# Optimization experiments

Measured on AMD Instinct MI355X. Metric: run time of the kernel, lower is better.

The kernel has to match this reference:

```python
import jax, jax.numpy as jnp
import numpy as np

N = 8192
IN_DIM = 512
OUT_DIM = 256
ALPHA = 0.2  # LeakyReLU negative slope


def setup_inputs() -> dict:
    key = jax.random.key(0)
    k_nodes, k_edge, k_W, k_Wb, k_a1, k_a1b, k_a2, k_a2b = jax.random.split(key, 8)
    nodes = jax.random.normal(k_nodes, (N, IN_DIM), dtype=jnp.float32)
    edge_mat = jax.random.uniform(k_edge, (N, N)) > 0.5
    edge_mat = edge_mat | jnp.eye(N, dtype=bool)
    s_W = 1.0 / np.sqrt(IN_DIM)
    s_a = 1.0 / np.sqrt(OUT_DIM)
    W_w = jax.random.uniform(k_W, (OUT_DIM, IN_DIM), minval=-s_W, maxval=s_W, dtype=jnp.float32)
    W_b = jax.random.uniform(k_Wb, (OUT_DIM,), minval=-s_W, maxval=s_W, dtype=jnp.float32)
    a1_w = jax.random.uniform(k_a1, (1, OUT_DIM), minval=-s_a, maxval=s_a, dtype=jnp.float32)
    a1_b = jax.random.uniform(k_a1b, (1,), minval=-s_a, maxval=s_a, dtype=jnp.float32)
    a2_w = jax.random.uniform(k_a2, (1, OUT_DIM), minval=-s_a, maxval=s_a, dtype=jnp.float32)
    a2_b = jax.random.uniform(k_a2b, (1,), minval=-s_a, maxval=s_a, dtype=jnp.float32)
    return {"nodes": nodes, "edge_mat": edge_mat, "W_w": W_w, "W_b": W_b,
            "a1_w": a1_w, "a1_b": a1_b, "a2_w": a2_w, "a2_b": a2_b}


def reference(nodes, edge_mat, W_w, W_b, a1_w, a1_b, a2_w, a2_b):
    Wh = nodes @ W_w.T + W_b                      # [N, OUT_DIM]
    Wh1 = Wh @ a1_w.T + a1_b                      # [N, 1]
    Wh2 = Wh @ a2_w.T + a2_b                      # [N, 1]
    scores = jax.nn.leaky_relu(Wh1 + Wh2.T, negative_slope=ALPHA)  # [N, N]
    masked = jnp.where(edge_mat, scores, -jnp.inf)
    attention = jax.nn.softmax(masked, axis=1)    # [N, N]
    return attention @ Wh                         # [N, OUT_DIM]
```

## Files before the change

kernel.cpp:

```cpp
#include <hip/hip_runtime.h>
#include <hip/hip_bf16.h>
#include <stdint.h>


#define NN 8192
#define IND 512
#define OUTD 256

typedef __attribute__((ext_vector_type(8))) short short8;
typedef __attribute__((ext_vector_type(4))) short short4v;
typedef __attribute__((ext_vector_type(4))) float f32x4;
typedef __attribute__((ext_vector_type(4))) int i32x4;
typedef __attribute__((ext_vector_type(4))) unsigned int u32x4;

#define AS_GLOBAL __attribute__((address_space(1)))
#define AS_LDS __attribute__((address_space(3)))

static __device__ __forceinline__ short f2bf(float f) {
  return __builtin_bit_cast(short, __float2bfloat16(f));
}

extern "C" __global__ __launch_bounds__(256) void k_convert_w(
    const float* __restrict__ W, short* __restrict__ W2) {
  const int t = blockIdx.x * 256 + threadIdx.x;
  const int row = t >> 6, kb = t & 63;
  const float* src = W + row * IND + kb * 8;
  f32x4 x0 = *(const f32x4*)src;
  f32x4 x1 = *(const f32x4*)(src + 4);
  short8 o;
  o[0] = f2bf(x0[0]); o[1] = f2bf(x0[1]); o[2] = f2bf(x0[2]); o[3] = f2bf(x0[3]);
  o[4] = f2bf(x1[0]); o[5] = f2bf(x1[1]); o[6] = f2bf(x1[2]); o[7] = f2bf(x1[3]);
  *(short8*)(W2 + (size_t)kb * 2048 + row * 8) = o;
}

extern "C" __global__ __launch_bounds__(128) void k_wh(
    const float* __restrict__ nodes, const short* __restrict__ W2,
    const float* __restrict__ Wb, const float* __restrict__ a1w,
    const float* __restrict__ a1b, const float* __restrict__ a2w,
    const float* __restrict__ a2b, short* __restrict__ WhL,
    float* __restrict__ s1, float* __restrict__ sAC,
    uint32_t* __restrict__ sPK) {
  const int tid = threadIdx.x;
  const int wv = tid >> 6, lane = tid & 63, g = lane >> 4, m = lane & 15;
  const int rowbase = blockIdx.x * 32 + wv * 16;

  f32x4 acc[16];
#pragma unroll
  for (int nf = 0; nf < 16; ++nf) acc[nf] = (f32x4){0.f, 0.f, 0.f, 0.f};

  const float* arow = nodes + (size_t)(rowbase + m) * IND;
  const short* bb = W2 + (size_t)g * 2048 + m * 8;
#pragma unroll 4
  for (int k0 = 0; k0 < IND; k0 += 32) {
    const float* ap = arow + k0 + g * 8;
    f32x4 x0 = *(const f32x4*)ap;
    f32x4 x1 = *(const f32x4*)(ap + 4);
    short8 af;
    af[0] = f2bf(x0[0]); af[1] = f2bf(x0[1]); af[2] = f2bf(x0[2]); af[3] = f2bf(x0[3]);
    af[4] = f2bf(x1[0]); af[5] = f2bf(x1[1]); af[6] = f2bf(x1[2]); af[7] = f2bf(x1[3]);
    const short* bk = bb + (size_t)(k0 >> 3) * 2048;
#pragma unroll
    for (int nf = 0; nf < 16; ++nf) {
      short8 bf = *(const short8*)(bk + nf * 128);
      acc[nf] = __builtin_amdgcn_mfma_f32_16x16x32_bf16(af, bf, acc[nf], 0, 0, 0);
    }
  }

  float p1[4] = {0.f, 0.f, 0.f, 0.f}, p2[4] = {0.f, 0.f, 0.f, 0.f};
#pragma unroll
  for (int nf = 0; nf < 16; ++nf) {
    const int n = nf * 16 + m;
    const float b = Wb[n], c1 = a1w[n], c2 = a2w[n];
#pragma unroll
    for (int r = 0; r < 4; ++r) {
      float v = acc[nf][r] + b;
      acc[nf][r] = v;
      p1[r] += c1 * v;
      p2[r] += c2 * v;
    }
  }
#pragma unroll
  for (int off = 1; off < 16; off <<= 1) {
#pragma unroll
    for (int r = 0; r < 4; ++r) {
      p1[r] += __shfl_xor(p1[r], off);
      p2[r] += __shfl_xor(p2[r], off);
    }
  }
  if (m == 0) {
    const float b1 = a1b[0], b2 = a2b[0];
#pragma unroll
    for (int r = 0; r < 4; ++r) {
      const int row = rowbase + g * 4 + r;
      const float v1 = p1[r] + b1, v2 = p2[r] + b2;
      s1[row] = v1;
      sAC[row] = __expf(v1);
      sAC[NN + row] = __expf(0.2f * v1);
      const float B = __expf(v2), D = __expf(0.2f * v2);
      sPK[2 * row] = __builtin_bit_cast(uint32_t, B);
      sPK[2 * row + 1] =
          ((uint32_t)(uint16_t)f2bf(D) << 16) | (uint16_t)f2bf(v2);
    }
  }

  const size_t cbase = ((size_t)(rowbase >> 3) + (g >> 1)) * 2048 + (g & 1) * 4;
#pragma unroll
  for (int nf = 0; nf < 16; ++nf) {
    short4v o;
#pragma unroll
    for (int r = 0; r < 4; ++r) o[r] = f2bf(acc[nf][r]);
    *(short4v*)(WhL + cbase + (size_t)(nf * 16 + m) * 8) = o;
  }
}

extern "C" __global__ __launch_bounds__(512, 4) void k_attn(
    const int* __restrict__ mask, const short* __restrict__ WhL,
    const float* __restrict__ s1, const float* __restrict__ sAC,
    const uint32_t* __restrict__ sPK,
    float* __restrict__ pnum, float* __restrict__ pden) {
  __shared__ char smem[51200];
  uint32_t* PKs = (uint32_t*)(smem + 32768);
  char* Ms = smem + 40960;

  const int tid = threadIdx.x;
  const int w = tid >> 6, lane = tid & 63, g = lane >> 4, m = lane & 15;
  const int rt = blockIdx.x >> 3, jc = blockIdx.x & 7;
  const int rg = w & 3, ns = w >> 2;
  const int rb = rt * 128 + rg * 32;

  const float T0 = -s1[rb + m],        T1 = -s1[rb + 16 + m];
  const float A0 = sAC[rb + m],        A1 = sAC[rb + 16 + m];
  const float C0 = sAC[NN + rb + m],   C1 = sAC[NN + rb + 16 + m];

  f32x4 acc0[8], acc1[8];
#pragma unroll
  for (int nf = 0; nf < 8; ++nf) {
    acc0[nf] = (f32x4){0.f, 0.f, 0.f, 0.f};
    acc1[nf] = (f32x4){0.f, 0.f, 0.f, 0.f};
  }
  float den0 = 0.f, den1 = 0.f;

  const int rloc = tid >> 2, jq = tid & 3;
  const int* msrc = mask + (size_t)(rt * 128 + rloc) * NN + jc * 1024 + jq * 8;
  const int mwr = rloc * 40 + jq * 8;
  const int mrow0 = (rg * 32 + m) * 40 + g * 8;
  const int mrow1 = (rg * 32 + 16 + m) * 40 + g * 8;
  const short* gS = WhL + (size_t)jc * 262144;

  auto pack8 = [](const i32x4& a, const i32x4& b) -> uint64_t {
    uint64_t p = 0;
    p |= (a[0] != 0) ? 1ull : 0;
    p |= (a[1] != 0) ? (1ull << 8) : 0;
    p |= (a[2] != 0) ? (1ull << 16) : 0;
    p |= (a[3] != 0) ? (1ull << 24) : 0;
    p |= (b[0] != 0) ? (1ull << 32) : 0;
    p |= (b[1] != 0) ? (1ull << 40) : 0;
    p |= (b[2] != 0) ? (1ull << 48) : 0;
    p |= (b[3] != 0) ? (1ull << 56) : 0;
    return p;
  };

  auto build = [&](float T, float A, float C, uint64_t pb,
                   const u32x4& q0, const u32x4& q1,
                   const u32x4& q2, const u32x4& q3, float& den) -> short8 {
    const uint32_t Bv[8] = {q0[0], q0[2], q1[0], q1[2],
                            q2[0], q2[2], q3[0], q3[2]};
    const uint32_t Dv[8] = {q0[1], q0[3], q1[1], q1[3],
                            q2[1], q2[3], q3[1], q3[3]};
    short8 af;
#pragma unroll
    for (int i = 0; i < 8; ++i) {
      const float s2v = __builtin_bit_cast(float, Dv[i] << 16);
      const bool pos = s2v > T;
      const float wv = __builtin_bit_cast(float, pos ? Bv[i] : (Dv[i] & 0xFFFF0000u));
      const float a = pos ? A : C;
      const float val = wv * a;
      const float pv = ((pb >> (8 * i)) & 1) ? val : 0.f;
      den += pv;
      af[i] = f2bf(pv);
    }
    return af;
  };

  i32x4 mA0 = __builtin_nontemporal_load((const i32x4*)msrc);
  i32x4 mA1 = __builtin_nontemporal_load((const i32x4*)(msrc + 4));
  __builtin_amdgcn_global_load_lds(
      (const AS_GLOBAL void*)((const char*)sPK + (size_t)jc * 8192 + tid * 16),
      (AS_LDS void*)(smem + 32768 + tid * 16), 16, 0, 0);
  __builtin_amdgcn_global_load_lds((const AS_GLOBAL void*)(gS + tid * 8),
                                   (AS_LDS void*)(smem + tid * 16), 16, 0, 0);
  __builtin_amdgcn_global_load_lds((const AS_GLOBAL void*)(gS + 4096 + tid * 8),
                                   (AS_LDS void*)(smem + 8192 + tid * 16), 16, 0, 0);
  *(uint64_t*)(Ms + mwr) = pack8(mA0, mA1);
  i32x4 mB0 = __builtin_nontemporal_load((const i32x4*)(msrc + 32));
  i32x4 mB1 = __builtin_nontemporal_load((const i32x4*)(msrc + 36));
  asm volatile("s_waitcnt vmcnt(2)" ::: "memory");
  __builtin_amdgcn_sched_barrier(0);
  asm volatile("s_waitcnt lgkmcnt(0)" ::: "memory");
  __builtin_amdgcn_s_barrier();

  auto body = [&](int u, i32x4& is0, i32x4& is1, i32x4& cs0, i32x4& cs1) {
    const int wn = (u + 2 < 32) ? u + 2 : 31;
    is0 = __builtin_nontemporal_load((const i32x4*)(msrc + wn * 32));
    is1 = __builtin_nontemporal_load((const i32x4*)(msrc + wn * 32 + 4));
    const int us = (u + 1 < 32) ? u + 1 : 31;
    {
      const short* gsl = gS + us * 8192 + tid * 8;
      char* dst = smem + ((u + 1) & 1) * 16384 + tid * 16;
      __builtin_amdgcn_global_load_lds((const AS_GLOBAL void*)gsl,
                                       (AS_LDS void*)dst, 16, 0, 0);
      __builtin_amdgcn_global_load_lds((const AS_GLOBAL void*)(gsl + 4096),
                                       (AS_LDS void*)(dst + 8192), 16, 0, 0);
    }
    asm volatile("s_waitcnt vmcnt(4)" ::: "memory");
    __builtin_amdgcn_sched_barrier(0);
    if (u < 31) *(uint64_t*)(Ms + ((u + 1) & 1) * 5120 + mwr) = pack8(cs0, cs1);
    const uint64_t pb0 = *(const uint64_t*)(Ms + (u & 1) * 5120 + mrow0);
    const uint64_t pb1 = *(const uint64_t*)(Ms + (u & 1) * 5120 + mrow1);
    const uint32_t* pk = &PKs[u * 64 + g * 16];
    const u32x4 q0 = *(const u32x4*)(pk + 0);
    const u32x4 q1 = *(const u32x4*)(pk + 4);
    const u32x4 q2 = *(const u32x4*)(pk + 8);
    const u32x4 q3 = *(const u32x4*)(pk + 12);
    short8 af0 = build(T0, A0, C0, pb0, q0, q1, q2, q3, den0);
    short8 af1 = build(T1, A1, C1, pb1, q0, q1, q2, q3, den1);
    const short* bl = (const short*)(smem + (u & 1) * 16384) +
                      g * 2048 + (ns * 128 + m) * 8;
#pragma unroll
    for (int nf = 0; nf < 8; ++nf) {
      short8 bf = *(const short8*)(bl + nf * 128);
      acc0[nf] = __builtin_amdgcn_mfma_f32_16x16x32_bf16(af0, bf, acc0[nf], 0, 0, 0);
      acc1[nf] = __builtin_amdgcn_mfma_f32_16x16x32_bf16(af1, bf, acc1[nf], 0, 0, 0);
    }
    asm volatile("s_waitcnt lgkmcnt(0)" ::: "memory");
    __builtin_amdgcn_s_barrier();
  };

  for (int uu = 0; uu < 32; uu += 2) {
    body(uu, mA0, mA1, mB0, mB1);
    body(uu + 1, mB0, mB1, mA0, mA1);
  }

  den0 += __shfl_xor(den0, 16); den0 += __shfl_xor(den0, 32);
  den1 += __shfl_xor(den1, 16); den1 += __shfl_xor(den1, 32);
  if (ns == 0 && lane < 16) {
    pden[jc * NN + rb + m] = den0;
    pden[jc * NN + rb + 16 + m] = den1;
  }

  float* pn = pnum + (size_t)jc * NN * OUTD + (size_t)rb * OUTD + ns * 128;
#pragma unroll
  for (int r = 0; r < 4; ++r) {
    const int q = g * 4 + r;
#pragma unroll
    for (int nf = 0; nf < 8; ++nf) {
      pn[(size_t)q * OUTD + nf * 16 + m] = acc0[nf][r];
      pn[(size_t)(16 + q) * OUTD + nf * 16 + m] = acc1[nf][r];
    }
  }
}

extern "C" __global__ __launch_bounds__(256) void k_comb(
    const float* __restrict__ pnum, const float* __restrict__ pden,
    float* __restrict__ out) {
  const int idx = blockIdx.x * 256 + threadIdx.x;
  const int row = idx >> 6, c4 = (idx & 63) * 4;
  f32x4 s = (f32x4){0.f, 0.f, 0.f, 0.f};
  float d = 0.f;
#pragma unroll
  for (int jc = 0; jc < 8; ++jc) {
    f32x4 v = *(const f32x4*)(pnum + ((size_t)jc * NN + row) * OUTD + c4);
    s += v;
    d += pden[jc * NN + row];
  }
  const float inv = 1.f / d;
  *(f32x4*)(out + (size_t)row * OUTD + c4) = s * inv;
}

extern "C" void kernel_launch(void* const* d_in, const int* in_sizes, int n_in,
                              void* d_out, int out_size, void* d_ws, size_t ws_size,
                              hipStream_t stream) {
  const float* nodes = (const float*)d_in[0];
  const int*   mask  = (const int*)d_in[1];
  const float* W_w   = (const float*)d_in[2];
  const float* W_b   = (const float*)d_in[3];
  const float* a1w   = (const float*)d_in[4];
  const float* a1b   = (const float*)d_in[5];
  const float* a2w   = (const float*)d_in[6];
  const float* a2b   = (const float*)d_in[7];
  float* out = (float*)d_out;

  char* ws = (char*)d_ws;
  short*    WhL  = (short*)(ws);
  float*    s1   = (float*)(ws + (size_t)4  * 1024 * 1024);
  short*    W2   = (short*)(ws + (size_t)4  * 1024 * 1024 + 65536);
  float*    sAC  = (float*)(ws + (size_t)13 * 1024 * 1024);
  uint32_t* sPK  = (uint32_t*)(ws + (size_t)14 * 1024 * 1024);
  float*    pnum = (float*)(ws + (size_t)16 * 1024 * 1024);
  float*    pden = (float*)(ws + (size_t)96 * 1024 * 1024);

  hipLaunchKernelGGL(k_convert_w, dim3(64), dim3(256), 0, stream, W_w, W2);
  hipLaunchKernelGGL(k_wh, dim3(256), dim3(128), 0, stream,
                     nodes, W2, W_b, a1w, a1b, a2w, a2b, WhL, s1, sAC, sPK);
  hipLaunchKernelGGL(k_attn, dim3(512), dim3(512), 0, stream,
                     mask, WhL, s1, sAC, sPK, pnum, pden);
  hipLaunchKernelGGL(k_comb, dim3(2048), dim3(256), 0, stream,
                     pnum, pden, out);
}
```

Baseline: 198.6 us.

## Halve attention row tile and read mask directly into registers, drop LDS mask packing

The attention kernel now covers 64 rows per block instead of 128, with one 16-row MFMA fragment per wave. The grid doubles to 1024 blocks. Each lane loads its own mask ints straight from global memory into registers, which removes the LDS bit-packing stage and its extra barrier wait. The mask prefetch moves after the MFMAs, and the MFMA section runs at raised wave priority. The cost is that each block reads its WhL tiles from LDS for half as many rows, so WhL global/LDS traffic per output roughly doubles, and the mask loads are less coalesced.

```diff
diff --git a/kernel.cpp b/kernel.cpp
--- a/kernel.cpp
+++ b/kernel.cpp
@@ -118,51 +118,30 @@
     const float* __restrict__ s1, const float* __restrict__ sAC,
     const uint32_t* __restrict__ sPK,
     float* __restrict__ pnum, float* __restrict__ pden) {
-  __shared__ char smem[51200];
+  __shared__ char smem[40960];
   uint32_t* PKs = (uint32_t*)(smem + 32768);
-  char* Ms = smem + 40960;
 
   const int tid = threadIdx.x;
   const int w = tid >> 6, lane = tid & 63, g = lane >> 4, m = lane & 15;
   const int rt = blockIdx.x >> 3, jc = blockIdx.x & 7;
   const int rg = w & 3, ns = w >> 2;
-  const int rb = rt * 128 + rg * 32;
-
-  const float T0 = -s1[rb + m],        T1 = -s1[rb + 16 + m];
-  const float A0 = sAC[rb + m],        A1 = sAC[rb + 16 + m];
-  const float C0 = sAC[NN + rb + m],   C1 = sAC[NN + rb + 16 + m];
-
-  f32x4 acc0[8], acc1[8];
-#pragma unroll
-  for (int nf = 0; nf < 8; ++nf) {
-    acc0[nf] = (f32x4){0.f, 0.f, 0.f, 0.f};
-    acc1[nf] = (f32x4){0.f, 0.f, 0.f, 0.f};
-  }
-  float den0 = 0.f, den1 = 0.f;
-
-  const int rloc = tid >> 2, jq = tid & 3;
-  const int* msrc = mask + (size_t)(rt * 128 + rloc) * NN + jc * 1024 + jq * 8;
-  const int mwr = rloc * 40 + jq * 8;
-  const int mrow0 = (rg * 32 + m) * 40 + g * 8;
-  const int mrow1 = (rg * 32 + 16 + m) * 40 + g * 8;
+  const int rb = rt * 64 + rg * 16;
+
+  const float T0 = -s1[rb + m];
+  const float A0 = sAC[rb + m];
+  const float C0 = sAC[NN + rb + m];
+
+  f32x4 acc[8];
+#pragma unroll
+  for (int nf = 0; nf < 8; ++nf) acc[nf] = (f32x4){0.f, 0.f, 0.f, 0.f};
+  float den = 0.f;
+
+  const int* mr = mask + (size_t)(rb + m) * NN + jc * 1024 + g * 8;
   const short* gS = WhL + (size_t)jc * 262144;
 
-  auto pack8 = [](const i32x4& a, const i32x4& b) -> uint64_t {
-    uint64_t p = 0;
-    p |= (a[0] != 0) ? 1ull : 0;
-    p |= (a[1] != 0) ? (1ull << 8) : 0;
-    p |= (a[2] != 0) ? (1ull << 16) : 0;
-    p |= (a[3] != 0) ? (1ull << 24) : 0;
-    p |= (b[0] != 0) ? (1ull << 32) : 0;
-    p |= (b[1] != 0) ? (1ull << 40) : 0;
-    p |= (b[2] != 0) ? (1ull << 48) : 0;
-    p |= (b[3] != 0) ? (1ull << 56) : 0;
-    return p;
-  };
-
-  auto build = [&](float T, float A, float C, uint64_t pb,
+  auto build = [&](const i32x4& lo, const i32x4& hi,
                    const u32x4& q0, const u32x4& q1,
-                   const u32x4& q2, const u32x4& q3, float& den) -> short8 {
+                   const u32x4& q2, const u32x4& q3) -> short8 {
     const uint32_t Bv[8] = {q0[0], q0[2], q1[0], q1[2],
                             q2[0], q2[2], q3[0], q3[2]};
     const uint32_t Dv[8] = {q0[1], q0[3], q1[1], q1[3],
@@ -171,19 +150,22 @@
 #pragma unroll
     for (int i = 0; i < 8; ++i) {
       const float s2v = __builtin_bit_cast(float, Dv[i] << 16);
-      const bool pos = s2v > T;
+      const bool pos = s2v > T0;
       const float wv = __builtin_bit_cast(float, pos ? Bv[i] : (Dv[i] & 0xFFFF0000u));
-      const float a = pos ? A : C;
+      const float a = pos ? A0 : C0;
       const float val = wv * a;
-      const float pv = ((pb >> (8 * i)) & 1) ? val : 0.f;
+      const int mv = (i < 4) ? lo[i] : hi[i - 4];
+      const float pv = (mv != 0) ? val : 0.f;
       den += pv;
       af[i] = f2bf(pv);
     }
     return af;
   };
 
-  i32x4 mA0 = __builtin_nontemporal_load((const i32x4*)msrc);
-  i32x4 mA1 = __builtin_nontemporal_load((const i32x4*)(msrc + 4));
+  i32x4 mA0 = __builtin_nontemporal_load((const i32x4*)mr);
+  i32x4 mA1 = __builtin_nontemporal_load((const i32x4*)(mr + 4));
+  i32x4 mB0 = __builtin_nontemporal_load((const i32x4*)(mr + 32));
+  i32x4 mB1 = __builtin_nontemporal_load((const i32x4*)(mr + 36));
   __builtin_amdgcn_global_load_lds(
       (const AS_GLOBAL void*)((const char*)sPK + (size_t)jc * 8192 + tid * 16),
       (AS_LDS void*)(smem + 32768 + tid * 16), 16, 0, 0);
@@ -191,20 +173,12 @@
                                    (AS_LDS void*)(smem + tid * 16), 16, 0, 0);
   __builtin_amdgcn_global_load_lds((const AS_GLOBAL void*)(gS + 4096 + tid * 8),
                                    (AS_LDS void*)(smem + 8192 + tid * 16), 16, 0, 0);
-  *(uint64_t*)(Ms + mwr) = pack8(mA0, mA1);
-  i32x4 mB0 = __builtin_nontemporal_load((const i32x4*)(msrc + 32));
-  i32x4 mB1 = __builtin_nontemporal_load((const i32x4*)(msrc + 36));
-  asm volatile("s_waitcnt vmcnt(2)" ::: "memory");
-  __builtin_amdgcn_sched_barrier(0);
-  asm volatile("s_waitcnt lgkmcnt(0)" ::: "memory");
+  asm volatile("s_waitcnt vmcnt(0)" ::: "memory");
   __builtin_amdgcn_s_barrier();
 
-  auto body = [&](int u, i32x4& is0, i32x4& is1, i32x4& cs0, i32x4& cs1) {
-    const int wn = (u + 2 < 32) ? u + 2 : 31;
-    is0 = __builtin_nontemporal_load((const i32x4*)(msrc + wn * 32));
-    is1 = __builtin_nontemporal_load((const i32x4*)(msrc + wn * 32 + 4));
-    const int us = (u + 1 < 32) ? u + 1 : 31;
+  auto body = [&](int u, i32x4& c0, i32x4& c1) {
     {
+      const int us = (u + 1 < 32) ? u + 1 : 31;
       const short* gsl = gS + us * 8192 + tid * 8;
       char* dst = smem + ((u + 1) & 1) * 16384 + tid * 16;
       __builtin_amdgcn_global_load_lds((const AS_GLOBAL void*)gsl,
@@ -214,39 +188,37 @@
     }
     asm volatile("s_waitcnt vmcnt(4)" ::: "memory");
     __builtin_amdgcn_sched_barrier(0);
-    if (u < 31) *(uint64_t*)(Ms + ((u + 1) & 1) * 5120 + mwr) = pack8(cs0, cs1);
-    const uint64_t pb0 = *(const uint64_t*)(Ms + (u & 1) * 5120 + mrow0);
-    const uint64_t pb1 = *(const uint64_t*)(Ms + (u & 1) * 5120 + mrow1);
     const uint32_t* pk = &PKs[u * 64 + g * 16];
     const u32x4 q0 = *(const u32x4*)(pk + 0);
     const u32x4 q1 = *(const u32x4*)(pk + 4);
     const u32x4 q2 = *(const u32x4*)(pk + 8);
     const u32x4 q3 = *(const u32x4*)(pk + 12);
-    short8 af0 = build(T0, A0, C0, pb0, q0, q1, q2, q3, den0);
-    short8 af1 = build(T1, A1, C1, pb1, q0, q1, q2, q3, den1);
+    short8 af = build(c0, c1, q0, q1, q2, q3);
     const short* bl = (const short*)(smem + (u & 1) * 16384) +
                       g * 2048 + (ns * 128 + m) * 8;
+    __builtin_amdgcn_s_setprio(1);
 #pragma unroll
     for (int nf = 0; nf < 8; ++nf) {
       short8 bf = *(const short8*)(bl + nf * 128);
-      acc0[nf] = __builtin_amdgcn_mfma_f32_16x16x32_bf16(af0, bf, acc0[nf], 0, 0, 0);
-      acc1[nf] = __builtin_amdgcn_mfma_f32_16x16x32_bf16(af1, bf, acc1[nf], 0, 0, 0);
-    }
-    asm volatile("s_waitcnt lgkmcnt(0)" ::: "memory");
+      acc[nf] = __builtin_amdgcn_mfma_f32_16x16x32_bf16(af, bf, acc[nf], 0, 0, 0);
+    }
+    __builtin_amdgcn_s_setprio(0);
+    {
+      const int wn = (u + 2 < 32) ? u + 2 : 31;
+      c0 = __builtin_nontemporal_load((const i32x4*)(mr + wn * 32));
+      c1 = __builtin_nontemporal_load((const i32x4*)(mr + wn * 32 + 4));
+    }
     __builtin_amdgcn_s_barrier();
   };
 
   for (int uu = 0; uu < 32; uu += 2) {
-    body(uu, mA0, mA1, mB0, mB1);
-    body(uu + 1, mB0, mB1, mA0, mA1);
-  }
-
-  den0 += __shfl_xor(den0, 16); den0 += __shfl_xor(den0, 32);
-  den1 += __shfl_xor(den1, 16); den1 += __shfl_xor(den1, 32);
-  if (ns == 0 && lane < 16) {
-    pden[jc * NN + rb + m] = den0;
-    pden[jc * NN + rb + 16 + m] = den1;
-  }
+    body(uu, mA0, mA1);
+    body(uu + 1, mB0, mB1);
+  }
+
+  den += __shfl_xor(den, 16);
+  den += __shfl_xor(den, 32);
+  if (ns == 0 && lane < 16) pden[jc * NN + rb + m] = den;
 
   float* pn = pnum + (size_t)jc * NN * OUTD + (size_t)rb * OUTD + ns * 128;
 #pragma unroll
@@ -254,8 +226,7 @@
     const int q = g * 4 + r;
 #pragma unroll
     for (int nf = 0; nf < 8; ++nf) {
-      pn[(size_t)q * OUTD + nf * 16 + m] = acc0[nf][r];
-      pn[(size_t)(16 + q) * OUTD + nf * 16 + m] = acc1[nf][r];
+      pn[(size_t)q * OUTD + nf * 16 + m] = acc[nf][r];
     }
   }
 }
@@ -302,7 +273,7 @@
   hipLaunchKernelGGL(k_convert_w, dim3(64), dim3(256), 0, stream, W_w, W2);
   hipLaunchKernelGGL(k_wh, dim3(256), dim3(128), 0, stream,
                      nodes, W2, W_b, a1w, a1b, a2w, a2b, WhL, s1, sAC, sPK);
-  hipLaunchKernelGGL(k_attn, dim3(512), dim3(512), 0, stream,
+  hipLaunchKernelGGL(k_attn, dim3(1024), dim3(512), 0, stream,
                      mask, WhL, s1, sAC, sPK, pnum, pden);
   hipLaunchKernelGGL(k_comb, dim3(2048), dim3(256), 0, stream,
                      pnum, pden, out);
```

Result: slower. 203.4 us (+2.4%).
